# Kernel optimization log

Hardware: AMD Instinct MI355X
Metric: run time of the kernel (lower is better)

The kernel has to match this reference:

```python
import jax, jax.numpy as jnp
import numpy as np

B, C, H, W = 32, 512, 112, 112
RC = 32          # reduction_channels = 512 // 16
CPG = C // RC    # channels per group = 16
K, STRIDE, PAD = 3, 2, 1


def setup_inputs() -> dict:
    key = jax.random.key(0)
    ks = jax.random.split(key, 7)
    x = jax.random.normal(ks[0], (B, C, H, W), dtype=jnp.float32)
    # grouped conv weights: OIHW with I = in_channels // groups
    theta_w = jax.random.normal(ks[1], (RC, CPG, K, K), dtype=jnp.float32) * 0.05
    theta_b = jax.random.normal(ks[2], (RC,), dtype=jnp.float32) * 0.05
    phi_w = jax.random.normal(ks[3], (RC, CPG, K, K), dtype=jnp.float32) * 0.05
    phi_b = jax.random.normal(ks[4], (RC,), dtype=jnp.float32) * 0.05
    fc_w = jax.random.normal(ks[5], (RC, CPG, 1, 1), dtype=jnp.float32) * 0.05
    fc_b = jax.random.normal(ks[6], (RC,), dtype=jnp.float32) * 0.05
    return {"x": x, "theta_w": theta_w, "theta_b": theta_b,
            "phi_w": phi_w, "phi_b": phi_b, "fc_w": fc_w, "fc_b": fc_b}


def _gconv(x, w, b, stride, pad):
    groups = x.shape[1] // w.shape[1]
    y = jax.lax.conv_general_dilated(
        x, w, window_strides=(stride, stride),
        padding=[(pad, pad), (pad, pad)],
        dimension_numbers=("NCHW", "OIHW", "NCHW"),
        feature_group_count=groups)
    return y + b[None, :, None, None]


def reference(x, theta_w, theta_b, phi_w, phi_b, fc_w, fc_b):
    b = x.shape[0]
    theta = _gconv(x, theta_w, theta_b, STRIDE, PAD)          # [B,RC,56,56]
    rc = theta.shape[1]
    theta = theta.reshape(b, rc, -1)                          # [B,RC,S]
    phi = _gconv(x, phi_w, phi_b, STRIDE, PAD).reshape(b, rc, -1)  # [B,RC,S]
    # global average pool + grouped 1x1 fc (stride irrelevant on 1x1 input)
    gap = jnp.mean(x, axis=(2, 3))                            # [B,C]
    g = jnp.einsum("bgk,gk->bg", gap.reshape(b, rc, -1), fc_w[:, :, 0, 0]) + fc_b  # [B,RC]
    # channel-channel attention: theta @ phi^T -> softmax -> @ g
    mat = jnp.einsum("bcs,bds->bcd", theta, phi)              # [B,RC,RC]
    mat = jax.nn.softmax(mat, axis=-1)
    out = jnp.einsum("bcd,bd->bc", mat, g)                    # [B,RC]
    return out[:, :, None, None]                              # [B,RC,1,1]
```

## Files before the change

### kernel.cpp

```cpp
#include <hip/hip_runtime.h>

#define BATCH 32
#define CIN   512
#define H     112
#define W     112
#define RC    32
#define CPG   16
#define HO    56
#define WO    56
#define S     3136
#define TY    4
#define NTILE 14
#define SC    16
#define CH    196
#define CHP   204

#define WS_THETA 0
#define WS_PHI   (RC*BATCH*S)
#define WS_GAP   (2*RC*BATCH*S)
#define WS_MAT   (WS_GAP + BATCH*CIN)

__global__ __launch_bounds__(256)
void conv_gap_kernel(const float* __restrict__ x,
                     const float* __restrict__ thw, const float* __restrict__ thb,
                     const float* __restrict__ phw, const float* __restrict__ phb,
                     float* __restrict__ theta_out, float* __restrict__ phi_out,
                     float* __restrict__ gapsum)
{
    const int ty  = blockIdx.x;
    const int g   = blockIdx.y;
    const int b   = blockIdx.z;
    const int tid = threadIdx.x;

    __shared__ float wth[CPG*9], wph[CPG*9];
    if (tid < CPG*9) {
        wth[tid] = thw[g*(CPG*9) + tid];
        wph[tid] = phw[g*(CPG*9) + tid];
    }
    __syncthreads();

    const float* xg = x + (size_t)(b*CIN + g*CPG) * (H*W);

    if (tid < WO*TY) {
        const int ox = tid % WO;
        const int oy = ty*TY + tid / WO;
        float at = thb[g];
        float ap = phb[g];
        const int iy0 = 2*oy - 1;
        const int ix0 = 2*ox - 1;
        for (int i = 0; i < CPG; ++i) {
            const float* xc = xg + i*(H*W);
            #pragma unroll
            for (int ky = 0; ky < 3; ++ky) {
                const int iy = iy0 + ky;
                if ((unsigned)iy < (unsigned)H) {
                    const float* row = xc + iy*W;
                    #pragma unroll
                    for (int kx = 0; kx < 3; ++kx) {
                        const int ix = ix0 + kx;
                        if ((unsigned)ix < (unsigned)W) {
                            const float v = row[ix];
                            at = fmaf(v, wth[i*9 + ky*3 + kx], at);
                            ap = fmaf(v, wph[i*9 + ky*3 + kx], ap);
                        }
                    }
                }
            }
        }
        const size_t o = (size_t)(b*RC + g)*S + oy*WO + ox;
        theta_out[o] = at;
        phi_out[o]  = ap;
    }

    {
        const int c = tid >> 4;
        const int j = tid & 15;
        const float* xc = xg + c*(H*W) + (8*ty)*W;
        float ssum = 0.f;
        for (int e = j; e < 8*W; e += 16) ssum += xc[e];
        #pragma unroll
        for (int off = 8; off; off >>= 1) ssum += __shfl_down(ssum, off, 16);
        if (j == 0) atomicAdd(&gapsum[b*CIN + g*CPG + c], ssum);
    }
}

__global__ __launch_bounds__(256)
void mat_kernel(const float* __restrict__ theta, const float* __restrict__ phi,
                float* __restrict__ matpart)
{
    const int sc  = blockIdx.x;
    const int b   = blockIdx.y;
    const int tid = threadIdx.x;

    __shared__ float th_s[RC*CHP];
    __shared__ float ph_s[RC*CHP];

    const size_t gbase = (size_t)b*RC*S + (size_t)sc*CH;
    for (int idx = tid; idx < RC*CH; idx += 256) {
        const int c = idx / CH;
        const int s = idx - c*CH;
        th_s[c*CHP + s] = theta[gbase + (size_t)c*S + s];
        ph_s[c*CHP + s] = phi[gbase + (size_t)c*S + s];
    }
    __syncthreads();

    const int cpair = tid >> 4;
    const int dpair = tid & 15;
    const int c0 = 2*cpair, c1 = c0 + 1;
    const int d0 = 2*dpair, d1 = d0 + 1;

    float a00 = 0.f, a01 = 0.f, a10 = 0.f, a11 = 0.f;
    for (int s4 = 0; s4 < CH; s4 += 4) {
        const float4 ta = *(const float4*)(th_s + c0*CHP + s4);
        const float4 tb = *(const float4*)(th_s + c1*CHP + s4);
        const float4 pa = *(const float4*)(ph_s + d0*CHP + s4);
        const float4 pb = *(const float4*)(ph_s + d1*CHP + s4);
        a00 += ta.x*pa.x + ta.y*pa.y + ta.z*pa.z + ta.w*pa.w;
        a01 += ta.x*pb.x + ta.y*pb.y + ta.z*pb.z + ta.w*pb.w;
        a10 += tb.x*pa.x + tb.y*pa.y + tb.z*pa.z + tb.w*pa.w;
        a11 += tb.x*pb.x + tb.y*pb.y + tb.z*pb.z + tb.w*pb.w;
    }
    float* mp = matpart + ((size_t)b*SC + sc)*(RC*RC);
    mp[c0*RC + d0] = a00;
    mp[c0*RC + d1] = a01;
    mp[c1*RC + d0] = a10;
    mp[c1*RC + d1] = a11;
}

__global__ __launch_bounds__(64)
void final_kernel(const float* __restrict__ matpart, const float* __restrict__ gapsum,
                  const float* __restrict__ fcw, const float* __restrict__ fcb,
                  float* __restrict__ out)
{
    const int b   = blockIdx.x;
    const int tid = threadIdx.x;
    __shared__ float m_s[RC*33];
    __shared__ float g_s[RC];

    for (int idx = tid; idx < RC*RC; idx += 64) {
        float s = 0.f;
        const float* mp = matpart + (size_t)b*SC*RC*RC + idx;
        #pragma unroll
        for (int sc = 0; sc < SC; ++sc) s += mp[sc*RC*RC];
        m_s[(idx >> 5)*33 + (idx & 31)] = s;
    }
    if (tid < RC) {
        const float* gp = gapsum + b*CIN + tid*CPG;
        const float* wp = fcw + tid*CPG;
        float acc = 0.f;
        for (int i = 0; i < CPG; ++i) acc += gp[i]*wp[i];
        g_s[tid] = fcb[tid] + acc * (1.0f/(float)(H*W));
    }
    __syncthreads();
    if (tid < RC) {
        const float* row = m_s + tid*33;
        float m = -1e30f;
        for (int d = 0; d < RC; ++d) m = fmaxf(m, row[d]);
        float se = 0.f, num = 0.f;
        for (int d = 0; d < RC; ++d) {
            const float e = expf(row[d] - m);
            se  += e;
            num += e * g_s[d];
        }
        out[b*RC + tid] = num / se;
    }
}

extern "C" void kernel_launch(void* const* d_in, const int* in_sizes, int n_in,
                              void* d_out, int out_size, void* d_ws, size_t ws_size,
                              hipStream_t stream)
{
    const float* x   = (const float*)d_in[0];
    const float* thw = (const float*)d_in[1];
    const float* thb = (const float*)d_in[2];
    const float* phw = (const float*)d_in[3];
    const float* phb = (const float*)d_in[4];
    const float* fcw = (const float*)d_in[5];
    const float* fcb = (const float*)d_in[6];
    float* out = (float*)d_out;
    float* ws  = (float*)d_ws;

    float* theta = ws + WS_THETA;
    float* phi   = ws + WS_PHI;
    float* gap   = ws + WS_GAP;
    float* mat   = ws + WS_MAT;

    hipMemsetAsync(gap, 0, BATCH*CIN*sizeof(float), stream);
    conv_gap_kernel<<<dim3(NTILE, RC, BATCH), 256, 0, stream>>>(
        x, thw, thb, phw, phb, theta, phi, gap);
    mat_kernel<<<dim3(SC, BATCH), 256, 0, stream>>>(theta, phi, mat);
    final_kernel<<<BATCH, 64, 0, stream>>>(mat, gap, fcw, fcb, out);
}
```

Baseline: 1.330 ms.

## Fuse grouped conv, GAP/fc and Gram matrix into one tiled kernel

Merges the conv+GAP kernel and the theta·phi^T kernel into a single kernel per (row tile, batch). Each block streams all 512 channels through a double-buffered shared-memory row tile with register prefetch, computes both convolutions, folds the fc weights into the GAP partial sums, and forms partial Gram matrices from shared memory. This removes the theta/phi round trip through global memory, the memset and the atomics. The cost is a much smaller grid (448 blocks) with one barrier per channel, so latency hiding and occupancy may suffer.

```diff
diff --git a/kernel.cpp b/kernel.cpp
--- a/kernel.cpp
+++ b/kernel.cpp
@@ -2,154 +2,173 @@
 
 #define BATCH 32
 #define CIN   512
-#define H     112
-#define W     112
+#define HH    112
+#define WW    112
 #define RC    32
 #define CPG   16
 #define HO    56
 #define WO    56
-#define S     3136
 #define TY    4
 #define NTILE 14
-#define SC    16
-#define CH    196
-#define CHP   204
-
-#define WS_THETA 0
-#define WS_PHI   (RC*BATCH*S)
-#define WS_GAP   (2*RC*BATCH*S)
-#define WS_MAT   (WS_GAP + BATCH*CIN)
-
-__global__ __launch_bounds__(256)
-void conv_gap_kernel(const float* __restrict__ x,
-                     const float* __restrict__ thw, const float* __restrict__ thb,
-                     const float* __restrict__ phw, const float* __restrict__ phb,
-                     float* __restrict__ theta_out, float* __restrict__ phi_out,
-                     float* __restrict__ gapsum)
+#define SPT   (TY*WO)
+#define XROWS 9
+#define XW    120
+#define TSP   228
+#define HW    (HH*WW)
+
+#define WS_MAT 0
+#define WS_GAP (BATCH*NTILE*RC*RC)
+
+__device__ __forceinline__ float4 ldx(const float* p, bool pred) {
+    float4 v = make_float4(0.f, 0.f, 0.f, 0.f);
+    if (pred) v = *(const float4*)p;
+    return v;
+}
+
+__global__ __launch_bounds__(256, 2)
+void conv_gram_kernel(const float* __restrict__ x,
+                      const float* __restrict__ thw, const float* __restrict__ thb,
+                      const float* __restrict__ phw, const float* __restrict__ phb,
+                      const float* __restrict__ fcw,
+                      float* __restrict__ matpart, float* __restrict__ gpart)
 {
-    const int ty  = blockIdx.x;
-    const int g   = blockIdx.y;
-    const int b   = blockIdx.z;
-    const int tid = threadIdx.x;
-
-    __shared__ float wth[CPG*9], wph[CPG*9];
-    if (tid < CPG*9) {
-        wth[tid] = thw[g*(CPG*9) + tid];
-        wph[tid] = phw[g*(CPG*9) + tid];
-    }
-    __syncthreads();
-
-    const float* xg = x + (size_t)(b*CIN + g*CPG) * (H*W);
-
-    if (tid < WO*TY) {
-        const int ox = tid % WO;
-        const int oy = ty*TY + tid / WO;
-        float at = thb[g];
-        float ap = phb[g];
-        const int iy0 = 2*oy - 1;
-        const int ix0 = 2*ox - 1;
-        for (int i = 0; i < CPG; ++i) {
-            const float* xc = xg + i*(H*W);
-            #pragma unroll
-            for (int ky = 0; ky < 3; ++ky) {
-                const int iy = iy0 + ky;
-                if ((unsigned)iy < (unsigned)H) {
-                    const float* row = xc + iy*W;
-                    #pragma unroll
-                    for (int kx = 0; kx < 3; ++kx) {
-                        const int ix = ix0 + kx;
-                        if ((unsigned)ix < (unsigned)W) {
-                            const float v = row[ix];
-                            at = fmaf(v, wth[i*9 + ky*3 + kx], at);
-                            ap = fmaf(v, wph[i*9 + ky*3 + kx], ap);
-                        }
-                    }
-                }
-            }
-        }
-        const size_t o = (size_t)(b*RC + g)*S + oy*WO + ox;
-        theta_out[o] = at;
-        phi_out[o]  = ap;
-    }
-
-    {
-        const int c = tid >> 4;
-        const int j = tid & 15;
-        const float* xc = xg + c*(H*W) + (8*ty)*W;
-        float ssum = 0.f;
-        for (int e = j; e < 8*W; e += 16) ssum += xc[e];
-        #pragma unroll
-        for (int off = 8; off; off >>= 1) ssum += __shfl_down(ssum, off, 16);
-        if (j == 0) atomicAdd(&gapsum[b*CIN + g*CPG + c], ssum);
-    }
-}
-
-__global__ __launch_bounds__(256)
-void mat_kernel(const float* __restrict__ theta, const float* __restrict__ phi,
-                float* __restrict__ matpart)
-{
-    const int sc  = blockIdx.x;
+    const int t   = blockIdx.x;
     const int b   = blockIdx.y;
     const int tid = threadIdx.x;
 
-    __shared__ float th_s[RC*CHP];
-    __shared__ float ph_s[RC*CHP];
-
-    const size_t gbase = (size_t)b*RC*S + (size_t)sc*CH;
-    for (int idx = tid; idx < RC*CH; idx += 256) {
-        const int c = idx / CH;
-        const int s = idx - c*CH;
-        th_s[c*CHP + s] = theta[gbase + (size_t)c*S + s];
-        ph_s[c*CHP + s] = phi[gbase + (size_t)c*S + s];
-    }
+    __shared__ __align__(16) float xs[2][XROWS*XW];
+    __shared__ __align__(16) float th_s[RC*TSP];
+    __shared__ __align__(16) float ph_s[RC*TSP];
+    __shared__ float g_red[4*RC];
+
+    for (int r = tid; r < XROWS; r += 256) {
+        #pragma unroll
+        for (int k = 0; k < 4; ++k) {
+            xs[0][r*XW + k] = 0.f;       xs[1][r*XW + k] = 0.f;
+            xs[0][r*XW + 116 + k] = 0.f; xs[1][r*XW + 116 + k] = 0.f;
+        }
+    }
+
+    const bool sact = tid < 252;
+    const int  srow = (4*tid) / WW;
+    const int  scol = (4*tid) % WW;
+    const bool oobz = (t == 0) && (srow == 0);
+    const bool ldp  = sact && !oobz;
+    const bool gapv = sact && (srow >= 1);
+    const float* xbase = x + (size_t)b*CIN*HW + (long)(8*t - 1 + srow)*WW + scol;
+    const int  sdst = srow*XW + 4 + scol;
+
+    const bool cact = tid < SPT;
+    const int  ry   = tid / WO;
+    const int  ox   = tid - ry*WO;
+    const int  cbase = (2*ry)*XW + 3 + 2*ox;
+
+    float4 v0 = ldx(xbase, ldp);
+    if (sact) *(float4*)(&xs[0][sdst]) = v0;
+    float gcur = gapv ? (v0.x + v0.y + v0.z + v0.w) * fcw[0] : 0.f;
+    float4 va = ldx(xbase + (size_t)1*HW, ldp);
+    float4 vb = ldx(xbase + (size_t)2*HW, ldp);
+
+    for (int g = 0; g < RC; ++g) {
+        float tacc = thb[g];
+        float pacc = phb[g];
+        #pragma unroll 4
+        for (int i = 0; i < CPG; ++i) {
+            const int ch = g*CPG + i;
+            float4 vn = make_float4(0.f, 0.f, 0.f, 0.f);
+            if (ch + 3 < CIN) vn = ldx(xbase + (size_t)(ch + 3)*HW, ldp);
+
+            __syncthreads();
+
+            if (cact) {
+                const float* xr = &xs[ch & 1][cbase];
+                const float* wt = thw + ch*9;
+                const float* wp = phw + ch*9;
+                const float a0 = xr[0],      a1 = xr[1],      a2 = xr[2];
+                const float b0 = xr[XW],     b1 = xr[XW+1],   b2 = xr[XW+2];
+                const float c0 = xr[2*XW],   c1 = xr[2*XW+1], c2 = xr[2*XW+2];
+                tacc = fmaf(a0, wt[0], tacc); pacc = fmaf(a0, wp[0], pacc);
+                tacc = fmaf(a1, wt[1], tacc); pacc = fmaf(a1, wp[1], pacc);
+                tacc = fmaf(a2, wt[2], tacc); pacc = fmaf(a2, wp[2], pacc);
+                tacc = fmaf(b0, wt[3], tacc); pacc = fmaf(b0, wp[3], pacc);
+                tacc = fmaf(b1, wt[4], tacc); pacc = fmaf(b1, wp[4], pacc);
+                tacc = fmaf(b2, wt[5], tacc); pacc = fmaf(b2, wp[5], pacc);
+                tacc = fmaf(c0, wt[6], tacc); pacc = fmaf(c0, wp[6], pacc);
+                tacc = fmaf(c1, wt[7], tacc); pacc = fmaf(c1, wp[7], pacc);
+                tacc = fmaf(c2, wt[8], tacc); pacc = fmaf(c2, wp[8], pacc);
+            }
+
+            if (i == CPG - 1) {
+                if (cact) { th_s[g*TSP + tid] = tacc; ph_s[g*TSP + tid] = pacc; }
+                float r = gcur;
+                #pragma unroll
+                for (int off = 32; off; off >>= 1) r += __shfl_down(r, off);
+                if ((tid & 63) == 0) g_red[(tid >> 6)*RC + g] = r;
+                gcur = 0.f;
+            }
+
+            if (ch + 1 < CIN) {
+                if (sact) *(float4*)(&xs[(ch + 1) & 1][sdst]) = va;
+                if (gapv) gcur = fmaf(va.x + va.y + va.z + va.w, fcw[ch + 1], gcur);
+                va = vb; vb = vn;
+            }
+        }
+    }
+
     __syncthreads();
 
-    const int cpair = tid >> 4;
-    const int dpair = tid & 15;
-    const int c0 = 2*cpair, c1 = c0 + 1;
-    const int d0 = 2*dpair, d1 = d0 + 1;
-
-    float a00 = 0.f, a01 = 0.f, a10 = 0.f, a11 = 0.f;
-    for (int s4 = 0; s4 < CH; s4 += 4) {
-        const float4 ta = *(const float4*)(th_s + c0*CHP + s4);
-        const float4 tb = *(const float4*)(th_s + c1*CHP + s4);
-        const float4 pa = *(const float4*)(ph_s + d0*CHP + s4);
-        const float4 pb = *(const float4*)(ph_s + d1*CHP + s4);
-        a00 += ta.x*pa.x + ta.y*pa.y + ta.z*pa.z + ta.w*pa.w;
-        a01 += ta.x*pb.x + ta.y*pb.y + ta.z*pb.z + ta.w*pb.w;
-        a10 += tb.x*pa.x + tb.y*pa.y + tb.z*pa.z + tb.w*pa.w;
-        a11 += tb.x*pb.x + tb.y*pb.y + tb.z*pb.z + tb.w*pb.w;
-    }
-    float* mp = matpart + ((size_t)b*SC + sc)*(RC*RC);
-    mp[c0*RC + d0] = a00;
-    mp[c0*RC + d1] = a01;
-    mp[c1*RC + d0] = a10;
-    mp[c1*RC + d1] = a11;
-}
-
-__global__ __launch_bounds__(64)
-void final_kernel(const float* __restrict__ matpart, const float* __restrict__ gapsum,
-                  const float* __restrict__ fcw, const float* __restrict__ fcb,
-                  float* __restrict__ out)
+    {
+        const int c  = tid >> 3;
+        const int dq = tid & 7;
+        const float* tr = th_s + c*TSP;
+        const float* p0 = ph_s + dq*TSP;
+        float a0 = 0.f, a1 = 0.f, a2 = 0.f, a3 = 0.f;
+        for (int s = 0; s < SPT; s += 4) {
+            const float4 tv = *(const float4*)(tr + s);
+            const float4 q0 = *(const float4*)(p0 + s);
+            const float4 q1 = *(const float4*)(p0 + 8*TSP + s);
+            const float4 q2 = *(const float4*)(p0 + 16*TSP + s);
+            const float4 q3 = *(const float4*)(p0 + 24*TSP + s);
+            a0 += tv.x*q0.x + tv.y*q0.y + tv.z*q0.z + tv.w*q0.w;
+            a1 += tv.x*q1.x + tv.y*q1.y + tv.z*q1.z + tv.w*q1.w;
+            a2 += tv.x*q2.x + tv.y*q2.y + tv.z*q2.z + tv.w*q2.w;
+            a3 += tv.x*q3.x + tv.y*q3.y + tv.z*q3.z + tv.w*q3.w;
+        }
+        float* mp = matpart + ((size_t)b*NTILE + t)*(RC*RC) + c*RC + dq;
+        mp[0]  = a0;
+        mp[8]  = a1;
+        mp[16] = a2;
+        mp[24] = a3;
+    }
+
+    if (tid < RC) {
+        const float s = g_red[tid] + g_red[RC + tid] + g_red[2*RC + tid] + g_red[3*RC + tid];
+        gpart[((size_t)b*NTILE + t)*RC + tid] = s;
+    }
+}
+
+__global__ __launch_bounds__(256)
+void final_kernel(const float* __restrict__ matpart, const float* __restrict__ gpart,
+                  const float* __restrict__ fcb, float* __restrict__ out)
 {
     const int b   = blockIdx.x;
     const int tid = threadIdx.x;
     __shared__ float m_s[RC*33];
     __shared__ float g_s[RC];
 
-    for (int idx = tid; idx < RC*RC; idx += 64) {
+    for (int idx = tid; idx < RC*RC; idx += 256) {
         float s = 0.f;
-        const float* mp = matpart + (size_t)b*SC*RC*RC + idx;
+        const float* mp = matpart + (size_t)b*NTILE*RC*RC + idx;
         #pragma unroll
-        for (int sc = 0; sc < SC; ++sc) s += mp[sc*RC*RC];
+        for (int tt = 0; tt < NTILE; ++tt) s += mp[tt*RC*RC];
         m_s[(idx >> 5)*33 + (idx & 31)] = s;
     }
     if (tid < RC) {
-        const float* gp = gapsum + b*CIN + tid*CPG;
-        const float* wp = fcw + tid*CPG;
-        float acc = 0.f;
-        for (int i = 0; i < CPG; ++i) acc += gp[i]*wp[i];
-        g_s[tid] = fcb[tid] + acc * (1.0f/(float)(H*W));
+        float s = 0.f;
+        const float* gp = gpart + (size_t)b*NTILE*RC + tid;
+        #pragma unroll
+        for (int tt = 0; tt < NTILE; ++tt) s += gp[tt*RC];
+        g_s[tid] = fcb[tid] + s * (1.0f/(float)HW);
     }
     __syncthreads();
     if (tid < RC) {
@@ -180,14 +199,10 @@
     float* out = (float*)d_out;
     float* ws  = (float*)d_ws;
 
-    float* theta = ws + WS_THETA;
-    float* phi   = ws + WS_PHI;
-    float* gap   = ws + WS_GAP;
-    float* mat   = ws + WS_MAT;
-
-    hipMemsetAsync(gap, 0, BATCH*CIN*sizeof(float), stream);
-    conv_gap_kernel<<<dim3(NTILE, RC, BATCH), 256, 0, stream>>>(
-        x, thw, thb, phw, phb, theta, phi, gap);
-    mat_kernel<<<dim3(SC, BATCH), 256, 0, stream>>>(theta, phi, mat);
-    final_kernel<<<BATCH, 64, 0, stream>>>(mat, gap, fcw, fcb, out);
-}
+    float* matpart = ws + WS_MAT;
+    float* gpart   = ws + WS_GAP;
+
+    conv_gram_kernel<<<dim3(NTILE, BATCH), 256, 0, stream>>>(
+        x, thw, thb, phw, phb, fcw, matpart, gpart);
+    final_kernel<<<BATCH, 256, 0, stream>>>(matpart, gpart, fcb, out);
+}
```

Measured after the change: 1.134 ms. 1.17x faster.
